# Performance work log

Measured on AMD Instinct MI355X. Metric: run time of the kernel, lower is better.

The kernel has to match this reference:

```python
import jax, jax.numpy as jnp
import numpy as np

NP, NA = 200000, 100000        # paper / author node counts
EW, EC = 300000, 300000        # writes / cites edge counts
HID, H, D = 128, 4, 32         # hidden, heads, head dim
FIN_P, FIN_A, OUT = 256, 128, 16
SCALE = float(1.0 / np.sqrt(D))


def _seg_softmax(alpha, idx, n):
    # softmax over edges grouped by destination node (PyG softmax)
    m = jax.ops.segment_max(alpha, idx, num_segments=n)
    e = jnp.exp(alpha - m[idx])
    s = jax.ops.segment_sum(e, idx, num_segments=n)
    return e / (s[idx] + 1e-16)


def _edge_type(k_src, v_src, q_dst, src, dst, a_rel, m_rel, p_rel, n_dst):
    # per-relation transform at node level, then gather-attend-scatter
    kr = jnp.einsum('nhd,hde->nhe', k_src, a_rel)
    vr = jnp.einsum('nhd,hde->nhe', v_src, m_rel)
    alpha = jnp.sum(q_dst[dst] * kr[src], axis=-1) * p_rel * SCALE  # [E,H]
    alpha = _seg_softmax(alpha, dst, n_dst)
    return jax.ops.segment_sum(vr[src] * alpha[..., None], dst, num_segments=n_dst)


def setup_inputs() -> dict:
    key = jax.random.key(0)
    ks = iter(jax.random.split(key, 48))

    def nrm(shape, s=0.05):
        return jax.random.normal(next(ks), shape, jnp.float32) * s

    inp = dict(
        x_paper=nrm((NP, FIN_P), 1.0),
        x_author=nrm((NA, FIN_A), 1.0),
        writes_src=jax.random.randint(next(ks), (EW,), 0, NA, dtype=jnp.int32),
        writes_dst=jax.random.randint(next(ks), (EW,), 0, NP, dtype=jnp.int32),
        cites_src=jax.random.randint(next(ks), (EC,), 0, NP, dtype=jnp.int32),
        cites_dst=jax.random.randint(next(ks), (EC,), 0, NP, dtype=jnp.int32),
        lin_paper_w=nrm((FIN_P, HID)), lin_paper_b=jnp.zeros((HID,), jnp.float32),
        lin_author_w=nrm((FIN_A, HID)), lin_author_b=jnp.zeros((HID,), jnp.float32),
        lin_out_w=nrm((HID, OUT)), lin_out_b=jnp.zeros((OUT,), jnp.float32),
    )
    for t in ('paper', 'author'):
        for nm in ('k', 'q', 'v', 'a'):
            inp[f'{nm}_w_{t}'] = nrm((HID, HID))
            inp[f'{nm}_b_{t}'] = jnp.zeros((HID,), jnp.float32)
        inp[f'skip_{t}'] = jnp.ones((), jnp.float32)
    for e in ('writes', 'cites'):
        inp[f'a_rel_{e}'] = nrm((H, D, D), 0.18)
        inp[f'm_rel_{e}'] = nrm((H, D, D), 0.18)
        inp[f'p_rel_{e}'] = jnp.ones((H,), jnp.float32)
    return inp


def reference(x_paper, x_author, writes_src, writes_dst, cites_src, cites_dst,
              lin_paper_w, lin_paper_b, lin_author_w, lin_author_b,
              lin_out_w, lin_out_b,
              k_w_paper, k_b_paper, q_w_paper, q_b_paper, v_w_paper, v_b_paper,
              a_w_paper, a_b_paper, skip_paper,
              k_w_author, k_b_author, q_w_author, q_b_author, v_w_author, v_b_author,
              a_w_author, a_b_author, skip_author,
              a_rel_writes, m_rel_writes, p_rel_writes,
              a_rel_cites, m_rel_cites, p_rel_cites):
    # per-node-type input projection + relu
    hp = jax.nn.relu(x_paper @ lin_paper_w + lin_paper_b)
    ha = jax.nn.relu(x_author @ lin_author_w + lin_author_b)
    # HGTConv: per-node-type k/q/v, [N,H,D]
    k_p = (hp @ k_w_paper + k_b_paper).reshape(NP, H, D)
    q_p = (hp @ q_w_paper + q_b_paper).reshape(NP, H, D)
    v_p = (hp @ v_w_paper + v_b_paper).reshape(NP, H, D)
    k_a = (ha @ k_w_author + k_b_author).reshape(NA, H, D)
    v_a = (ha @ v_w_author + v_b_author).reshape(NA, H, D)
    # heterogeneous multi-relation attention, group='sum' over edge types
    out_p = _edge_type(k_a, v_a, q_p, writes_src, writes_dst,
                       a_rel_writes, m_rel_writes, p_rel_writes, NP)
    out_p = out_p + _edge_type(k_p, v_p, q_p, cites_src, cites_dst,
                               a_rel_cites, m_rel_cites, p_rel_cites, NP)
    # output projection + gated skip (paper type; only 'paper' feeds the head)
    op = jax.nn.gelu(out_p.reshape(NP, HID), approximate=False) @ a_w_paper + a_b_paper
    beta = jax.nn.sigmoid(skip_paper)
    hp = beta * op + (1.0 - beta) * hp
    return hp @ lin_out_w + lin_out_b  # [NP, OUT]
```

## Files before the change

### kernel.cpp

```cpp
#include <hip/hip_runtime.h>
#include <cstdint>

#define NP 200000
#define NA 100000
#define EW 300000
#define EC 300000
#define HID 128
#define FIN_P 256
#define FIN_A 128
#define NOUT 16
#define ATT_SCALE 0.17677669529663687f

#define NBP 1563
#define NBA 782

#define SCAN_N (2 * NP)
#define SCAN_BS 256
#define SCAN_ITEMS 4
#define SCAN_TILE 1024
#define SCAN_NB ((SCAN_N + SCAN_TILE - 1) / SCAN_TILE)

typedef short s8v __attribute__((ext_vector_type(8)));
typedef float f32x4 __attribute__((ext_vector_type(4)));
typedef unsigned short ushort_t;

__device__ __forceinline__ float gelu_f(float x) {
  return 0.5f * x * (1.0f + erff(x * 0.70710678118654752f));
}
__device__ __forceinline__ ushort_t f2bf(float f) {
  unsigned u = __float_as_uint(f);
  return (ushort_t)((u + 0x7FFFu + ((u >> 16) & 1u)) >> 16);
}
__device__ __forceinline__ unsigned pack2bf(float a, float b) {
  return (unsigned)f2bf(a) | ((unsigned)f2bf(b) << 16);
}
__device__ __forceinline__ unsigned cvtpk(float a, float b) {
  unsigned r;
  asm("v_cvt_pk_bf16_f32 %0, %1, %2" : "=v"(r) : "v"(a), "v"(b));
  return r;
}
__device__ __forceinline__ float bflo(unsigned u) { return __uint_as_float(u << 16); }
__device__ __forceinline__ float bfhi(unsigned u) { return __uint_as_float(u & 0xFFFF0000u); }

__device__ __forceinline__ void gl16(const void* g, void* l) {
  __builtin_amdgcn_global_load_lds(
      (const __attribute__((address_space(1))) void*)g,
      (__attribute__((address_space(3))) void*)l, 16, 0, 0);
}

__device__ __forceinline__ int s2row(int r) { return (r ^ (r >> 2)) & 3; }

__global__ void prep_all(
    const float* __restrict__ qw,  const float* __restrict__ qb,
    const float* __restrict__ kwp, const float* __restrict__ kbp, const float* __restrict__ arc,
    const float* __restrict__ vwp, const float* __restrict__ vbp, const float* __restrict__ mrc,
    const float* __restrict__ kwa, const float* __restrict__ kba, const float* __restrict__ arw,
    const float* __restrict__ vwa, const float* __restrict__ vba, const float* __restrict__ mrw,
    const float* __restrict__ lpw, const float* __restrict__ law,
    const float* __restrict__ aw, const float* __restrict__ ab,
    const float* __restrict__ skip, const float* __restrict__ W2, const float* __restrict__ b2,
    ushort_t* __restrict__ Wall, float* __restrict__ Ball,
    ushort_t* __restrict__ Wcatb, float* __restrict__ bo,
    int* __restrict__ cnt)
{
  const int b = blockIdx.x, tid = threadIdx.x;
  if (b == 0) {
    for (int idx = tid; idx < 16384; idx += 256) {
      int c = idx >> 7, r = idx & 127;
      Wall[idx] = f2bf(qw[r * 128 + c]);
    }
    for (int c = tid; c < 128; c += 256) Ball[c] = qb[c];
  } else if (b <= 4) {
    const float *W, *bias, *rel;
    switch (b) {
      case 1:  W = kwp; bias = kbp; rel = arc; break;
      case 2:  W = vwp; bias = vbp; rel = mrc; break;
      case 3:  W = kwa; bias = kba; rel = arw; break;
      default: W = vwa; bias = vba; rel = mrw; break;
    }
    for (int idx = tid; idx < 16384; idx += 256) {
      int c = idx >> 7, r = idx & 127, h = c >> 5, e = c & 31;
      float s = 0.f;
      #pragma unroll
      for (int d = 0; d < 32; ++d) s += W[r * 128 + h * 32 + d] * rel[h * 1024 + d * 32 + e];
      Wall[b * 16384 + idx] = f2bf(s);
    }
    for (int c = tid; c < 128; c += 256) {
      int h = c >> 5, e = c & 31;
      float s = 0.f;
      #pragma unroll
      for (int d = 0; d < 32; ++d) s += bias[h * 32 + d] * rel[h * 1024 + d * 32 + e];
      Ball[b * 128 + c] = s;
    }
  } else if (b == 5) {
    for (int idx = tid; idx < 16384; idx += 256) {
      int c = idx >> 7, r = idx & 127;
      Wall[5 * 16384 + idx] = f2bf(law[r * 128 + c]);
    }
  } else if (b == 6) {
    for (int idx = tid; idx < 32768; idx += 256) {
      int c = idx >> 8, r = idx & 255;
      Wall[6 * 16384 + idx] = f2bf(lpw[r * 128 + c]);
    }
  } else if (b == 7) {
    float beta = 1.0f / (1.0f + expf(-skip[0]));
    for (int idx = tid; idx < 4096; idx += 256) {
      int c = idx >> 8, k = idx & 255;
      float v;
      if (k < 128) {
        float s = 0.f;
        for (int j = 0; j < 128; ++j) s += aw[k * 128 + j] * W2[j * 16 + c];
        v = beta * s;
      } else {
        v = (1.0f - beta) * W2[(k - 128) * 16 + c];
      }
      Wcatb[c * 256 + k] = f2bf(v);
    }
    if (tid < 16) {
      float s = 0.f;
      for (int k = 0; k < 128; ++k) s += ab[k] * W2[k * 16 + tid];
      bo[tid] = beta * s + b2[tid];
    }
  } else {
    int chunk = SCAN_N / 8;
    int base = (b - 8) * chunk;
    for (int i = tid; i < chunk; i += 256) cnt[base + i] = 0;
  }
}

__global__ __launch_bounds__(512) void gemm_main(
    const float* __restrict__ xp, const float* __restrict__ xa,
    const ushort_t* __restrict__ Wall,
    const float* __restrict__ bp, const float* __restrict__ ba,
    const float* __restrict__ Ball,
    ushort_t* __restrict__ hpo, ushort_t* __restrict__ hao,
    ushort_t* __restrict__ qkv, ushort_t* __restrict__ kvw)
{
  __shared__ ushort_t As[16384];
  __shared__ ushort_t Bs[16384];
  const bool isP = blockIdx.x < NBP;
  const int bid = isP ? blockIdx.x : blockIdx.x - NBP;
  const float* A = isP ? xp : xa;
  const ushort_t* Wp = Wall + (isP ? 6 * 16384 : 5 * 16384);
  const float* biasp = isP ? bp : ba;
  ushort_t* Chp = isP ? hpo : hao;
  const int M = isP ? NP : NA;
  const int KT = isP ? 256 : 128;
  const int nt = KT >> 6;
  const int base_set = isP ? 0 : 3;
  const int nsets = isP ? 3 : 2;

  const int tid  = threadIdx.x;
  const int lane = tid & 63;
  const int wv   = tid >> 6;
  const int wr   = wv >> 1, wc = wv & 1;
  const int l15  = lane & 15, kgl = lane >> 4;
  const int s2l  = (l15 ^ (l15 >> 2)) & 3;
  const int row0 = bid * 128;

  const int r0 = tid >> 2, kgp = tid & 3;
  const int sk = kgp ^ s2row(r0);
  int g0 = row0 + r0; if (g0 > M - 1) g0 = M - 1;

  {
    const float* a0p = A + (size_t)g0 * KT + sk * 8;
    const ushort_t* b0p = Wp + (size_t)r0 * KT + sk * 8;

    f32x4 acc[2][4];
    #pragma unroll
    for (int i = 0; i < 2; ++i)
      #pragma unroll
      for (int j = 0; j < 4; ++j) acc[i][j] = (f32x4){0.f, 0.f, 0.f, 0.f};

    for (int t = 0; t < nt; ++t) {
      const int kt = t * 64;
      gl16(b0p + kt,      &Bs[(size_t)tid * 8]);
      gl16(b0p + kt + 32, &Bs[(size_t)(tid + 512) * 8]);
      float4 fa0 = *(const float4*)(a0p + kt);
      float4 fa1 = *(const float4*)(a0p + kt + 4);
      float4 fb0 = *(const float4*)(a0p + kt + 32);
      float4 fb1 = *(const float4*)(a0p + kt + 36);
      uint4 v;
      v.x = cvtpk(fa0.x, fa0.y); v.y = cvtpk(fa0.z, fa0.w);
      v.z = cvtpk(fa1.x, fa1.y); v.w = cvtpk(fa1.z, fa1.w);
      *(uint4*)&As[(size_t)tid * 8] = v;
      v.x = cvtpk(fb0.x, fb0.y); v.y = cvtpk(fb0.z, fb0.w);
      v.z = cvtpk(fb1.x, fb1.y); v.w = cvtpk(fb1.z, fb1.w);
      *(uint4*)&As[(size_t)(tid + 512) * 8] = v;
      __syncthreads();

      const s8v* As8 = (const s8v*)As;
      const s8v* Bs8 = (const s8v*)Bs;
      #pragma unroll
      for (int pg = 0; pg < 2; ++pg) {
        s8v af[2], bfv[4];
        #pragma unroll
        for (int i = 0; i < 2; ++i)
          af[i]  = As8[pg * 512 + (wr * 32 + i * 16 + l15) * 4 + (kgl ^ s2l)];
        #pragma unroll
        for (int j = 0; j < 4; ++j)
          bfv[j] = Bs8[pg * 512 + (wc * 64 + j * 16 + l15) * 4 + (kgl ^ s2l)];
        #pragma unroll
        for (int i = 0; i < 2; ++i)
          #pragma unroll
          for (int j = 0; j < 4; ++j)
            acc[i][j] = __builtin_amdgcn_mfma_f32_16x16x32_bf16(af[i], bfv[j], acc[i][j], 0, 0, 0);
      }
      __syncthreads();
    }

    float bv[4];
    #pragma unroll
    for (int j = 0; j < 4; ++j) bv[j] = biasp[wc * 64 + j * 16 + l15];
    #pragma unroll
    for (int i = 0; i < 2; ++i) {
      #pragma unroll
      for (int r = 0; r < 4; ++r) {
        int row = wr * 32 + i * 16 + kgl * 4 + r;
        int o = ((row >> 2) & 3) << 3;
        #pragma unroll
        for (int j = 0; j < 4; ++j) {
          int col = wc * 64 + j * 16 + l15;
          float vv = acc[i][j][r] + bv[j];
          vv = fmaxf(vv, 0.f);
          int word = row * 64 + ((col >> 1) ^ o);
          Bs[word * 2 + (col & 1)] = f2bf(vv);
        }
      }
    }
    __syncthreads();
    {
      const unsigned* Cw = (const unsigned*)Bs;
      #pragma unroll
      for (int k = 0; k < 4; ++k) {
        int row = k * 32 + wv * 4 + (lane >> 4);
        int c16 = lane & 15;
        int word0 = row * 64 + ((c16 * 4) ^ (((row >> 2) & 3) << 3));
        uint4 vv = *(const uint4*)&Cw[word0];
        int grow = row0 + row;
        if (grow < M) *(uint4*)(Chp + (size_t)grow * 128 + c16 * 8) = vv;
      }
    }
  }
  __syncthreads();

  {
    const ushort_t* a0h = Chp + (size_t)g0 * 128 + sk * 8;
    #pragma unroll
    for (int t = 0; t < 4; ++t)
      gl16(a0h + t * 32, &As[((size_t)t * 512 + tid) * 8]);

    for (int si = 0; si < nsets; ++si) {
      const int set = base_set + si;
      const ushort_t* W = Wall + set * 16384;
      const float* bias = Ball + set * 128;
      ushort_t* C = isP ? (qkv + (size_t)set * NP * HID)
                        : (kvw + (size_t)(set - 3) * NA * HID);
      const ushort_t* b0p = W + (size_t)r0 * 128 + sk * 8;
      #pragma unroll
      for (int t = 0; t < 4; ++t)
        gl16(b0p + t * 32, &Bs[((size_t)t * 512 + tid) * 8]);
      __syncthreads();

      f32x4 acc[2][4];
      #pragma unroll
      for (int i = 0; i < 2; ++i)
        #pragma unroll
        for (int j = 0; j < 4; ++j) acc[i][j] = (f32x4){0.f, 0.f, 0.f, 0.f};

      const s8v* As8 = (const s8v*)As;
      const s8v* Bs8 = (const s8v*)Bs;
      #pragma unroll
      for (int t = 0; t < 4; ++t) {
        s8v af[2], bfv[4];
        #pragma unroll
        for (int i = 0; i < 2; ++i)
          af[i]  = As8[t * 512 + (wr * 32 + i * 16 + l15) * 4 + (kgl ^ s2l)];
        #pragma unroll
        for (int j = 0; j < 4; ++j)
          bfv[j] = Bs8[t * 512 + (wc * 64 + j * 16 + l15) * 4 + (kgl ^ s2l)];
        #pragma unroll
        for (int i = 0; i < 2; ++i)
          #pragma unroll
          for (int j = 0; j < 4; ++j)
            acc[i][j] = __builtin_amdgcn_mfma_f32_16x16x32_bf16(af[i], bfv[j], acc[i][j], 0, 0, 0);
      }
      __syncthreads();

      float bv[4];
      #pragma unroll
      for (int j = 0; j < 4; ++j) bv[j] = bias[wc * 64 + j * 16 + l15];
      #pragma unroll
      for (int i = 0; i < 2; ++i) {
        #pragma unroll
        for (int r = 0; r < 4; ++r) {
          int row = wr * 32 + i * 16 + kgl * 4 + r;
          int o = ((row >> 2) & 3) << 3;
          #pragma unroll
          for (int j = 0; j < 4; ++j) {
            int col = wc * 64 + j * 16 + l15;
            int word = row * 64 + ((col >> 1) ^ o);
            Bs[word * 2 + (col & 1)] = f2bf(acc[i][j][r] + bv[j]);
          }
        }
      }
      __syncthreads();
      {
        const unsigned* Cw = (const unsigned*)Bs;
        #pragma unroll
        for (int k = 0; k < 4; ++k) {
          int row = k * 32 + wv * 4 + (lane >> 4);
          int c16 = lane & 15;
          int word0 = row * 64 + ((c16 * 4) ^ (((row >> 2) & 3) << 3));
          uint4 vv = *(const uint4*)&Cw[word0];
          int grow = row0 + row;
          if (grow < M) *(uint4*)(C + (size_t)grow * 128 + c16 * 8) = vv;
        }
      }
      __syncthreads();
    }
  }
}

__global__ void hist_k(const int* __restrict__ wdst, const int* __restrict__ cdst,
                       int* __restrict__ cnt)
{
  int t = blockIdx.x * blockDim.x + threadIdx.x;
  if (t < EW) atomicAdd(&cnt[wdst[t]], 1);
  if (t < EC) atomicAdd(&cnt[NP + cdst[t]], 1);
}

__global__ __launch_bounds__(SCAN_BS) void scan1(const int* __restrict__ cnt,
                                                 int* __restrict__ off,
                                                 int* __restrict__ bsum)
{
  __shared__ int sh[2][SCAN_BS];
  int tid = threadIdx.x;
  int base = blockIdx.x * SCAN_TILE + tid * SCAN_ITEMS;
  int v[SCAN_ITEMS]; int tsum = 0;
  #pragma unroll
  for (int i = 0; i < SCAN_ITEMS; ++i) {
    int idx = base + i;
    v[i] = (idx < SCAN_N) ? cnt[idx] : 0;
    tsum += v[i];
  }
  int p = 0;
  sh[0][tid] = tsum; __syncthreads();
  #pragma unroll
  for (int d = 1; d < SCAN_BS; d <<= 1) {
    int x = sh[p][tid] + ((tid >= d) ? sh[p][tid - d] : 0);
    sh[p ^ 1][tid] = x; __syncthreads(); p ^= 1;
  }
  int run = sh[p][tid] - tsum;
  #pragma unroll
  for (int i = 0; i < SCAN_ITEMS; ++i) {
    int idx = base + i;
    if (idx < SCAN_N) off[idx] = run;
    run += v[i];
  }
  if (tid == SCAN_BS - 1) bsum[blockIdx.x] = sh[p][tid];
}

__global__ __launch_bounds__(512) void scan2(int* __restrict__ bsum)
{
  __shared__ int sh[2][512];
  int tid = threadIdx.x;
  int v = (tid < SCAN_NB) ? bsum[tid] : 0;
  int p = 0;
  sh[0][tid] = v; __syncthreads();
  for (int d = 1; d < 512; d <<= 1) {
    int x = sh[p][tid] + ((tid >= d) ? sh[p][tid - d] : 0);
    sh[p ^ 1][tid] = x; __syncthreads(); p ^= 1;
  }
  if (tid < SCAN_NB) bsum[tid] = sh[p][tid] - v;
}

__global__ __launch_bounds__(SCAN_BS) void scan3(int* __restrict__ off, int* __restrict__ cur,
                                                 const int* __restrict__ bsum)
{
  int add = bsum[blockIdx.x];
  int base = blockIdx.x * SCAN_TILE + threadIdx.x;
  #pragma unroll
  for (int i = 0; i < SCAN_ITEMS; ++i) {
    int idx = base + i * SCAN_BS;
    if (idx < SCAN_N) { int t = off[idx] + add; off[idx] = t; cur[idx] = t; }
  }
  if (blockIdx.x == 0 && threadIdx.x == 0) off[SCAN_N] = EW + EC;
}

__global__ void fill_k(const int* __restrict__ wsrc, const int* __restrict__ wdst,
                       const int* __restrict__ csrc, const int* __restrict__ cdst,
                       int* __restrict__ cur, int* __restrict__ esrc)
{
  int t = blockIdx.x * blockDim.x + threadIdx.x;
  if (t < EW) { int p = atomicAdd(&cur[wdst[t]], 1); esrc[p] = wsrc[t] << 8; }
  if (t < EC) { int p = atomicAdd(&cur[NP + cdst[t]], 1); esrc[p] = csrc[t] << 8; }
}

__global__ __launch_bounds__(256) void node_attn(
    const int* __restrict__ off, const int* __restrict__ esrc,
    const ushort_t* __restrict__ q,
    const ushort_t* __restrict__ kr_w, const ushort_t* __restrict__ vr_w,
    const ushort_t* __restrict__ kr_c, const ushort_t* __restrict__ vr_c,
    const float* __restrict__ p_rel_w, const float* __restrict__ p_rel_c,
    ushort_t* __restrict__ out_p)
{
  int gid = blockIdx.x * blockDim.x + threadIdx.x;
  int node = gid >> 4;
  int l16 = gid & 15;
  int h = l16 >> 2;
  unsigned loff = (unsigned)(l16 * 16);

  int eb0 = off[node],      ee0 = off[node + 1];
  int eb1 = off[NP + node], ee1 = off[NP + node + 1];

  uint4 qv = *(const uint4*)(q + (size_t)node * HID + l16 * 8);

  int i0a = (eb0 < ee0) ? eb0 : 0;
  int i0b = (eb0 + 1 < ee0) ? eb0 + 1 : 0;
  int i1a = (eb1 < ee1) ? eb1 : 0;
  int i1b = (eb1 + 1 < ee1) ? eb1 + 1 : 0;
  unsigned ba0 = (unsigned)esrc[i0a] + loff;
  unsigned bb0 = (unsigned)esrc[i0b] + loff;
  unsigned ba1 = (unsigned)esrc[i1a] + loff;
  unsigned bb1 = (unsigned)esrc[i1b] + loff;
  uint4 pka[2], pva[2], pkb[2], pvb[2];
  pka[0] = *(const uint4*)((const char*)kr_w + ba0);
  pva[0] = *(const uint4*)((const char*)vr_w + ba0);
  pkb[0] = *(const uint4*)((const char*)kr_w + bb0);
  pvb[0] = *(const uint4*)((const char*)vr_w + bb0);
  pka[1] = *(const uint4*)((const char*)kr_c + ba1);
  pva[1] = *(const uint4*)((const char*)vr_c + ba1);
  pkb[1] = *(const uint4*)((const char*)kr_c + bb1);
  pvb[1] = *(const uint4*)((const char*)vr_c + bb1);

  float qf[8];
  {
    const unsigned* pq = (const unsigned*)&qv;
    #pragma unroll
    for (int w = 0; w < 4; ++w) { qf[2 * w] = bflo(pq[w]); qf[2 * w + 1] = bfhi(pq[w]); }
  }
  float prw = p_rel_w[h] * ATT_SCALE;
  float prc = p_rel_c[h] * ATT_SCALE;

  float t[8];
  #pragma unroll
  for (int i = 0; i < 8; ++i) t[i] = 0.f;

  #pragma unroll
  for (int r = 0; r < 2; ++r) {
    const char* krb = (const char*)((r == 0) ? kr_w : kr_c);
    const char* vrb = (const char*)((r == 0) ? vr_w : vr_c);
    float prr = (r == 0) ? prw : prc;
    int eb = (r == 0) ? eb0 : eb1;
    int ee = (r == 0) ? ee0 : ee1;

    float s = 0.f;
    float A[8];
    #pragma unroll
    for (int i = 0; i < 8; ++i) A[i] = 0.f;

    int e = eb;
    #pragma unroll
    for (int pf = 0; pf < 2; ++pf) {
      if (e < ee) {
        const unsigned* k8 = (const unsigned*)((pf == 0) ? &pka[r] : &pkb[r]);
        const unsigned* v8 = (const unsigned*)((pf == 0) ? &pva[r] : &pvb[r]);
        float d = 0.f;
        #pragma unroll
        for (int w = 0; w < 4; ++w) {
          d = fmaf(qf[2 * w], bflo(k8[w]), d);
          d = fmaf(qf[2 * w + 1], bfhi(k8[w]), d);
        }
        d += __shfl_xor(d, 1);
        d += __shfl_xor(d, 2);
        float p = __expf(d * prr);
        s += p;
        #pragma unroll
        for (int w = 0; w < 4; ++w) {
          A[2 * w]     = fmaf(p, bflo(v8[w]), A[2 * w]);
          A[2 * w + 1] = fmaf(p, bfhi(v8[w]), A[2 * w + 1]);
        }
        ++e;
      }
    }
    for (; e < ee; ++e) {
      unsigned kb = (unsigned)esrc[e] + loff;
      uint4 kv = *(const uint4*)(krb + kb);
      uint4 vv = *(const uint4*)(vrb + kb);
      const unsigned* k8 = (const unsigned*)&kv;
      float d = 0.f;
      #pragma unroll
      for (int w = 0; w < 4; ++w) {
        d = fmaf(qf[2 * w], bflo(k8[w]), d);
        d = fmaf(qf[2 * w + 1], bfhi(k8[w]), d);
      }
      d += __shfl_xor(d, 1);
      d += __shfl_xor(d, 2);
      float p = __expf(d * prr);
      s += p;
      const unsigned* v8 = (const unsigned*)&vv;
      #pragma unroll
      for (int w = 0; w < 4; ++w) {
        A[2 * w]     = fmaf(p, bflo(v8[w]), A[2 * w]);
        A[2 * w + 1] = fmaf(p, bfhi(v8[w]), A[2 * w + 1]);
      }
    }
    float inv = 1.0f / (s + 1e-16f);
    #pragma unroll
    for (int i = 0; i < 8; ++i) t[i] = fmaf(A[i], inv, t[i]);
  }

  uint4 o;
  unsigned* po = (unsigned*)&o;
  #pragma unroll
  for (int w = 0; w < 4; ++w) po[w] = pack2bf(t[2 * w], t[2 * w + 1]);
  *(uint4*)(out_p + (size_t)node * HID + l16 * 8) = o;
}

__global__ __launch_bounds__(256) void epilogue_mfma(
    const ushort_t* __restrict__ out_p, const ushort_t* __restrict__ hp,
    const ushort_t* __restrict__ Wcatb, const float* __restrict__ bo,
    float* __restrict__ out)
{
  __shared__ ushort_t As[4096];
  const int tid  = threadIdx.x;
  const int lane = tid & 63;
  const int wv   = tid >> 6;
  const int l15  = lane & 15, kgl = lane >> 4;
  const int s2l  = (l15 ^ (l15 >> 2)) & 3;
  const int row0 = blockIdx.x * 128;

  const int r0 = tid >> 2, kgp = tid & 3;
  const int sk = kgp ^ s2row(r0);
  int g0 = row0 + r0;       if (g0 > NP - 1) g0 = NP - 1;
  int g1 = row0 + r0 + 64;  if (g1 > NP - 1) g1 = NP - 1;

  s8v bfr[8];
  #pragma unroll
  for (int ks = 0; ks < 8; ++ks)
    bfr[ks] = *(const s8v*)(Wcatb + (size_t)l15 * 256 + ks * 32 + kgl * 8);
  float bo_l = bo[l15];

  f32x4 acc[2];
  acc[0] = (f32x4){0.f, 0.f, 0.f, 0.f};
  acc[1] = (f32x4){0.f, 0.f, 0.f, 0.f};

  #pragma unroll
  for (int ph = 0; ph < 8; ++ph) {
    if (ph < 4) {
      const int kt = ph * 32;
      uint4 v0 = *(const uint4*)(out_p + (size_t)g0 * 128 + kt + sk * 8);
      uint4 v1 = *(const uint4*)(out_p + (size_t)g1 * 128 + kt + sk * 8);
      unsigned* p0 = (unsigned*)&v0;
      unsigned* p1 = (unsigned*)&v1;
      #pragma unroll
      for (int w = 0; w < 4; ++w) {
        p0[w] = cvtpk(gelu_f(bflo(p0[w])), gelu_f(bfhi(p0[w])));
        p1[w] = cvtpk(gelu_f(bflo(p1[w])), gelu_f(bfhi(p1[w])));
      }
      *(uint4*)&As[(size_t)tid * 8] = v0;
      *(uint4*)&As[(size_t)(tid + 256) * 8] = v1;
    } else {
      const int kt = (ph - 4) * 32;
      gl16(hp + (size_t)g0 * 128 + kt + sk * 8, &As[(size_t)tid * 8]);
      gl16(hp + (size_t)g1 * 128 + kt + sk * 8, &As[(size_t)(tid + 256) * 8]);
    }
    __syncthreads();

    const s8v* As8 = (const s8v*)As;
    s8v af0 = As8[(wv * 32 + l15) * 4 + (kgl ^ s2l)];
    s8v af1 = As8[(wv * 32 + 16 + l15) * 4 + (kgl ^ s2l)];
    acc[0] = __builtin_amdgcn_mfma_f32_16x16x32_bf16(af0, bfr[ph], acc[0], 0, 0, 0);
    acc[1] = __builtin_amdgcn_mfma_f32_16x16x32_bf16(af1, bfr[ph], acc[1], 0, 0, 0);
    __syncthreads();
  }

  #pragma unroll
  for (int i = 0; i < 2; ++i) {
    #pragma unroll
    for (int r = 0; r < 4; ++r) {
      int row = row0 + wv * 32 + i * 16 + kgl * 4 + r;
      if (row < NP) out[(size_t)row * NOUT + l15] = acc[i][r] + bo_l;
    }
  }
}

extern "C" void kernel_launch(void* const* d_in, const int* in_sizes, int n_in,
                              void* d_out, int out_size, void* d_ws, size_t ws_size,
                              hipStream_t stream)
{
  (void)in_sizes; (void)n_in; (void)out_size; (void)ws_size;
  const float* x_paper      = (const float*)d_in[0];
  const float* x_author     = (const float*)d_in[1];
  const int*   writes_src   = (const int*)d_in[2];
  const int*   writes_dst   = (const int*)d_in[3];
  const int*   cites_src    = (const int*)d_in[4];
  const int*   cites_dst    = (const int*)d_in[5];
  const float* lin_paper_w  = (const float*)d_in[6];
  const float* lin_paper_b  = (const float*)d_in[7];
  const float* lin_author_w = (const float*)d_in[8];
  const float* lin_author_b = (const float*)d_in[9];
  const float* lin_out_w    = (const float*)d_in[10];
  const float* lin_out_b    = (const float*)d_in[11];
  const float* k_w_paper    = (const float*)d_in[12];
  const float* k_b_paper    = (const float*)d_in[13];
  const float* q_w_paper    = (const float*)d_in[14];
  const float* q_b_paper    = (const float*)d_in[15];
  const float* v_w_paper    = (const float*)d_in[16];
  const float* v_b_paper    = (const float*)d_in[17];
  const float* a_w_paper    = (const float*)d_in[18];
  const float* a_b_paper    = (const float*)d_in[19];
  const float* skip_paper   = (const float*)d_in[20];
  const float* k_w_author   = (const float*)d_in[21];
  const float* k_b_author   = (const float*)d_in[22];
  const float* v_w_author   = (const float*)d_in[25];
  const float* v_b_author   = (const float*)d_in[26];
  const float* a_rel_writes = (const float*)d_in[30];
  const float* m_rel_writes = (const float*)d_in[31];
  const float* p_rel_writes = (const float*)d_in[32];
  const float* a_rel_cites  = (const float*)d_in[33];
  const float* m_rel_cites  = (const float*)d_in[34];
  const float* p_rel_cites  = (const float*)d_in[35];

  float* ws = (float*)d_ws;
  size_t off_f = 0;
  auto nxt = [&](size_t nfloats) { float* p = ws + off_f; off_f += nfloats; return p; };
  ushort_t* hp    = (ushort_t*)nxt((size_t)NP * 64);
  ushort_t* ha    = (ushort_t*)nxt((size_t)NA * 64);
  ushort_t* qkv   = (ushort_t*)nxt((size_t)3 * NP * 64);
  ushort_t* kvw   = (ushort_t*)nxt((size_t)2 * NA * 64);
  ushort_t* outp  = (ushort_t*)nxt((size_t)NP * 64);
  int*      cnt   = (int*)nxt(SCAN_N);
  int*      offs  = (int*)nxt(SCAN_N + 2);
  int*      cur   = (int*)nxt(SCAN_N);
  int*      esrc  = (int*)nxt(EW + EC);
  int*      bsum  = (int*)nxt(512);
  ushort_t* Wall  = (ushort_t*)nxt(65536);
  float*    Ball  = nxt(5 * 128);
  ushort_t* Wcatb = (ushort_t*)nxt(2048);
  float*    bo    = nxt(16);

  ushort_t* q_p  = qkv;
  ushort_t* kr_c = qkv + (size_t)NP * HID;
  ushort_t* vr_c = qkv + (size_t)2 * NP * HID;
  ushort_t* kr_w = kvw;
  ushort_t* vr_w = kvw + (size_t)NA * HID;

  prep_all<<<16, 256, 0, stream>>>(q_w_paper, q_b_paper,
                                   k_w_paper, k_b_paper, a_rel_cites,
                                   v_w_paper, v_b_paper, m_rel_cites,
                                   k_w_author, k_b_author, a_rel_writes,
                                   v_w_author, v_b_author, m_rel_writes,
                                   lin_paper_w, lin_author_w,
                                   a_w_paper, a_b_paper, skip_paper, lin_out_w, lin_out_b,
                                   Wall, Ball, Wcatb, bo, cnt);

  hist_k<<<(300000 + 255) / 256, 256, 0, stream>>>(writes_dst, cites_dst, cnt);
  scan1<<<SCAN_NB, SCAN_BS, 0, stream>>>(cnt, offs, bsum);
  scan2<<<1, 512, 0, stream>>>(bsum);
  scan3<<<SCAN_NB, SCAN_BS, 0, stream>>>(offs, cur, bsum);
  fill_k<<<(300000 + 255) / 256, 256, 0, stream>>>(writes_src, writes_dst,
                                                   cites_src, cites_dst, cur, esrc);

  gemm_main<<<NBP + NBA, 512, 0, stream>>>(x_paper, x_author, Wall,
                                           lin_paper_b, lin_author_b, Ball,
                                           hp, ha, qkv, kvw);

  node_attn<<<(NP * 16) / 256, 256, 0, stream>>>(
      offs, esrc, q_p, kr_w, vr_w, kr_c, vr_c, p_rel_writes, p_rel_cites, outp);

  epilogue_mfma<<<NBP, 256, 0, stream>>>(outp, hp, Wcatb, bo, (float*)d_out);
}
```

Measured before the change: 374.8 us.

## Double-buffer LDS tiles in projection GEMM to overlap loads with MFMA

Restructures the projection GEMM main loop into a two-stage LDS pipeline. Global loads for the next K-tile (the A floats into registers, the B tile via direct-to-LDS loads) are issued before the MFMAs on the current buffer. The A tile is converted to bf16 and written into the alternate buffer after compute, with one barrier per iteration instead of two. This is meant to hide global memory latency behind the matrix work, at the cost of twice the LDS footprint and hand-written waitcnt accounting that could be fragile.

New measurement: 374.6 us. No clear change (-0.1%).

```diff
diff --git a/kernel.cpp b/kernel.cpp
--- a/kernel.cpp
+++ b/kernel.cpp
@@ -172,14 +172,13 @@
       #pragma unroll
       for (int j = 0; j < 4; ++j) acc[i][j] = (f32x4){0.f, 0.f, 0.f, 0.f};
 
-    for (int t = 0; t < nt; ++t) {
-      const int kt = t * 64;
-      gl16(b0p + kt,      &Bs[(size_t)tid * 8]);
-      gl16(b0p + kt + 32, &Bs[(size_t)(tid + 512) * 8]);
-      float4 fa0 = *(const float4*)(a0p + kt);
-      float4 fa1 = *(const float4*)(a0p + kt + 4);
-      float4 fb0 = *(const float4*)(a0p + kt + 32);
-      float4 fb1 = *(const float4*)(a0p + kt + 36);
+    gl16(b0p,      &Bs[(size_t)tid * 8]);
+    gl16(b0p + 32, &Bs[(size_t)(tid + 512) * 8]);
+    {
+      float4 fa0 = *(const float4*)(a0p);
+      float4 fa1 = *(const float4*)(a0p + 4);
+      float4 fb0 = *(const float4*)(a0p + 32);
+      float4 fb1 = *(const float4*)(a0p + 36);
       uint4 v;
       v.x = cvtpk(fa0.x, fa0.y); v.y = cvtpk(fa0.z, fa0.w);
       v.z = cvtpk(fa1.x, fa1.y); v.w = cvtpk(fa1.z, fa1.w);
@@ -187,26 +186,60 @@
       v.x = cvtpk(fb0.x, fb0.y); v.y = cvtpk(fb0.z, fb0.w);
       v.z = cvtpk(fb1.x, fb1.y); v.w = cvtpk(fb1.z, fb1.w);
       *(uint4*)&As[(size_t)(tid + 512) * 8] = v;
-      __syncthreads();
+    }
+    asm volatile("s_waitcnt vmcnt(0) lgkmcnt(0)" ::: "memory");
+    __builtin_amdgcn_s_barrier();
+
+    int cur = 0;
+    for (int t = 0; t < nt; ++t) {
+      const bool more = (t + 1) < nt;
+      float4 ga0, ga1, gb0, gb1;
+      if (more) {
+        const int kn = (t + 1) * 64;
+        ga0 = *(const float4*)(a0p + kn);
+        ga1 = *(const float4*)(a0p + kn + 4);
+        gb0 = *(const float4*)(a0p + kn + 32);
+        gb1 = *(const float4*)(a0p + kn + 36);
+        const size_t nb = (size_t)(cur ^ 1) * 1024;
+        gl16(b0p + kn,      &Bs[(nb + tid) * 8]);
+        gl16(b0p + kn + 32, &Bs[(nb + 512 + tid) * 8]);
+        asm volatile("s_waitcnt vmcnt(6)" ::: "memory");
+      } else {
+        asm volatile("s_waitcnt vmcnt(0)" ::: "memory");
+      }
 
       const s8v* As8 = (const s8v*)As;
       const s8v* Bs8 = (const s8v*)Bs;
+      const int cb = cur * 1024;
       #pragma unroll
       for (int pg = 0; pg < 2; ++pg) {
         s8v af[2], bfv[4];
         #pragma unroll
         for (int i = 0; i < 2; ++i)
-          af[i]  = As8[pg * 512 + (wr * 32 + i * 16 + l15) * 4 + (kgl ^ s2l)];
+          af[i]  = As8[cb + pg * 512 + (wr * 32 + i * 16 + l15) * 4 + (kgl ^ s2l)];
         #pragma unroll
         for (int j = 0; j < 4; ++j)
-          bfv[j] = Bs8[pg * 512 + (wc * 64 + j * 16 + l15) * 4 + (kgl ^ s2l)];
+          bfv[j] = Bs8[cb + pg * 512 + (wc * 64 + j * 16 + l15) * 4 + (kgl ^ s2l)];
         #pragma unroll
         for (int i = 0; i < 2; ++i)
           #pragma unroll
           for (int j = 0; j < 4; ++j)
             acc[i][j] = __builtin_amdgcn_mfma_f32_16x16x32_bf16(af[i], bfv[j], acc[i][j], 0, 0, 0);
       }
-      __syncthreads();
+
+      if (more) {
+        const size_t nb = (size_t)(cur ^ 1) * 1024;
+        uint4 v;
+        v.x = cvtpk(ga0.x, ga0.y); v.y = cvtpk(ga0.z, ga0.w);
+        v.z = cvtpk(ga1.x, ga1.y); v.w = cvtpk(ga1.z, ga1.w);
+        *(uint4*)&As[(nb + tid) * 8] = v;
+        v.x = cvtpk(gb0.x, gb0.y); v.y = cvtpk(gb0.z, gb0.w);
+        v.z = cvtpk(gb1.x, gb1.y); v.w = cvtpk(gb1.z, gb1.w);
+        *(uint4*)&As[(nb + 512 + tid) * 8] = v;
+      }
+      asm volatile("s_waitcnt lgkmcnt(0)" ::: "memory");
+      __builtin_amdgcn_s_barrier();
+      cur ^= 1;
     }
 
     float bv[4];
```
